# Kernel tuning notes

Measured on AMD Instinct MI355X. Metric: run time of the kernel, lower is better.

Reference implementation:

```python
import jax, jax.numpy as jnp
import numpy as np

N_NODES = 100000
N_EDGES = 1000000
D_IN = 128
D_H = 128
N_CLS = 16


def setup_inputs() -> dict:
    key = jax.random.key(0)
    ks = jax.random.split(key, 12)
    s_in = 1.0 / np.sqrt(D_IN)
    s_h = 1.0 / np.sqrt(D_H)
    s_2h = 1.0 / np.sqrt(2 * D_H)
    return {
        "x": jax.random.normal(ks[0], (N_NODES, D_IN), jnp.float32),
        "edge_index": jax.random.randint(ks[1], (2, N_EDGES), 0, N_NODES, jnp.int64),
        "W_l0": jax.random.normal(ks[2], (D_H, D_IN), jnp.float32) * s_in,
        "b_l0": jnp.zeros((D_H,), jnp.float32),
        "W_r0": jax.random.normal(ks[3], (D_H, D_IN), jnp.float32) * s_in,
        "W_l1": jax.random.normal(ks[4], (D_H, D_H), jnp.float32) * s_h,
        "b_l1": jnp.zeros((D_H,), jnp.float32),
        "W_r1": jax.random.normal(ks[5], (D_H, D_H), jnp.float32) * s_h,
        "W_c": jax.random.normal(ks[6], (D_H, 2 * D_H), jnp.float32) * s_2h,
        "b_c": jnp.zeros((D_H,), jnp.float32),
        "W_o": jax.random.normal(ks[7], (N_CLS, 2 * D_H), jnp.float32) * s_2h,
        "b_o": jnp.zeros((N_CLS,), jnp.float32),
    }


def _sage_conv(x, src, dst, W_l, b_l, W_r, num_nodes):
    # PyG SAGEConv (mean aggr): lin_l(mean of source-neighbor feats) + lin_r(x)
    msgs = x[src]  # [E, d] gather
    agg = jax.ops.segment_sum(msgs, dst, num_segments=num_nodes)
    cnt = jax.ops.segment_sum(jnp.ones((src.shape[0],), x.dtype), dst, num_segments=num_nodes)
    mean = agg / jnp.maximum(cnt, 1.0)[:, None]
    return mean @ W_l.T + b_l + x @ W_r.T


def reference(x, edge_index, W_l0, b_l0, W_r0, W_l1, b_l1, W_r1, W_c, b_c, W_o, b_o):
    src, dst = edge_index[0], edge_index[1]
    n = x.shape[0]
    for W_l, b_l, W_r in ((W_l0, b_l0, W_r0), (W_l1, b_l1, W_r1)):
        x_old = x
        h = jax.nn.relu(_sage_conv(x, src, dst, W_l, b_l, W_r, n))
        x = jnp.concatenate([x_old, h], axis=-1)  # [N, 2*hidden]
        x = jax.nn.relu(x @ W_c.T + b_c)
        # dropout: identity (eval mode)
    edge_feats = jnp.concatenate([x[src], x[dst]], axis=-1)  # [E, 2*hidden]
    return edge_feats @ W_o.T + b_o
```

## Files before the change

kernel.cpp:

```cpp
#include <hip/hip_runtime.h>
#include <hip/hip_bf16.h>

#define NN 100000
#define NE 1000000
#define D  128
#define NC 16

typedef short short8 __attribute__((ext_vector_type(8)));
typedef float f32x4  __attribute__((ext_vector_type(4)));
typedef unsigned int u32x4 __attribute__((ext_vector_type(4)));

__device__ __forceinline__ float bf2f(ushort u) {
  union { unsigned int i; float f; } v; v.i = ((unsigned int)u) << 16; return v.f;
}
__device__ __forceinline__ ushort f2bf(float f) {
  union { float f; unsigned int i; } v; v.f = f;
  unsigned int x = v.i;
  return (ushort)((x + 0x7FFFu + ((x >> 16) & 1u)) >> 16);
}

#define BSH 9
#define NBKT ((NN + 511) >> BSH)
#define MS_NBLK 256
#define MS_EPB ((NE + MS_NBLK - 1) / MS_NBLK)
#define CSR_CAP 8192

__global__ void sniff_k(const ushort* __restrict__ xr, const unsigned int* __restrict__ ei,
                        int* __restrict__ flags, int* __restrict__ bhist) {
  int t = threadIdx.x;
  if (t < NBKT) bhist[t] = 0;
  if (t != 0 || blockIdx.x != 0) return;
  int f32 = 0;
  for (int i = 0; i < 128; ++i) {
    unsigned int e = ((unsigned int)xr[i] >> 7) & 0xFFu;
    if (e < 97u || e > 157u) f32 = 1;
  }
  flags[0] = f32;
  unsigned int s = 0;
  for (int i = 1; i < 256; i += 2) s |= ei[i];
  flags[1] = (s == 0) ? 1 : 0;
}

__global__ __launch_bounds__(256) void convert_idx_k(
    const int* __restrict__ ei, const int* __restrict__ flags,
    int* __restrict__ idx, int* __restrict__ bhist) {
  __shared__ int h[NBKT];
  for (int t = threadIdx.x; t < NBKT; t += 256) h[t] = 0;
  __syncthreads();
  const int stride = 256 * 256;
  const int i64 = flags[1];
  for (int i = blockIdx.x * 256 + threadIdx.x; i < 2 * NE; i += stride) {
    int v = i64 ? ei[2 * i] : ei[i];
    v = v < 0 ? 0 : (v >= NN ? NN - 1 : v);
    idx[i] = v;
    if (i >= NE) atomicAdd(&h[v >> BSH], 1);
  }
  __syncthreads();
  for (int t = threadIdx.x; t < NBKT; t += 256) if (h[t]) atomicAdd(&bhist[t], h[t]);
}

__global__ void convert_x_k(const void* __restrict__ xin, const int* __restrict__ flags,
                            ushort* __restrict__ xb) {
  int i = blockIdx.x * blockDim.x + threadIdx.x;
  const int n4 = NN * D / 4;
  if (i >= n4) return;
  ushort4 o;
  if (flags[0]) {
    float4 v = ((const float4*)xin)[i];
    o.x = f2bf(v.x); o.y = f2bf(v.y); o.z = f2bf(v.z); o.w = f2bf(v.w);
  } else {
    o = ((const ushort4*)xin)[i];
  }
  ((ushort4*)xb)[i] = o;
}

struct WPtrs { const void* p[10]; };
#define WTOT 102800
__global__ void convert_w_k(WPtrs w, const int* __restrict__ flags, ushort* __restrict__ wb) {
  const int off[10] = {0, 16384, 32768, 49152, 65536, 98304, 102400, 102528, 102656, 102784};
  int i = blockIdx.x * blockDim.x + threadIdx.x;
  if (i >= WTOT) return;
  int seg = 0;
  #pragma unroll
  for (int s2 = 1; s2 < 10; ++s2) if (i >= off[s2]) seg = s2;
  int j = i - off[seg];
  wb[i] = flags[0] ? f2bf(((const float*)w.p[seg])[j]) : ((const ushort*)w.p[seg])[j];
}

__global__ __launch_bounds__(256) void scanb_k(const int* __restrict__ bhist,
                                               int* __restrict__ bstart,
                                               int* __restrict__ bcur) {
  __shared__ int tmp[256];
  const int t = threadIdx.x;
  int v = (t < NBKT) ? bhist[t] : 0;
  tmp[t] = v;
  __syncthreads();
  for (int s = 1; s < 256; s <<= 1) {
    int u = (t >= s) ? tmp[t - s] : 0;
    __syncthreads();
    tmp[t] += u;
    __syncthreads();
  }
  if (t < NBKT) {
    int ex = tmp[t] - v;
    bstart[t] = ex;
    bcur[t] = ex;
  }
  if (t == NBKT - 1) bstart[NBKT] = tmp[t];
}

__global__ __launch_bounds__(512) void msplit_k(const int* __restrict__ src,
                                                const int* __restrict__ dst,
                                                int* __restrict__ bcur,
                                                int2* __restrict__ ebuf) {
  __shared__ int2 ep[MS_EPB];
  __shared__ int hist[NBKT];
  __shared__ int gbase[NBKT];
  const int e0 = blockIdx.x * MS_EPB;
  int n = NE - e0; if (n > MS_EPB) n = MS_EPB;
  for (int t = threadIdx.x; t < NBKT; t += 512) hist[t] = 0;
  __syncthreads();
  for (int t = threadIdx.x; t < n; t += 512) {
    int s = src[e0 + t], d = dst[e0 + t];
    ep[t] = make_int2(s, d);
    atomicAdd(&hist[d >> BSH], 1);
  }
  __syncthreads();
  for (int t = threadIdx.x; t < NBKT; t += 512) {
    gbase[t] = atomicAdd(&bcur[t], hist[t]);
    hist[t] = 0;
  }
  __syncthreads();
  for (int t = threadIdx.x; t < n; t += 512) {
    int2 p = ep[t];
    int b = p.y >> BSH;
    int loc = atomicAdd(&hist[b], 1);
    ebuf[gbase[b] + loc] = p;
  }
}

__global__ __launch_bounds__(512) void csr_k(const int2* __restrict__ ebuf,
                                             const int* __restrict__ bstart,
                                             int* __restrict__ off,
                                             int* __restrict__ nbr) {
  __shared__ int cnt_s[512];
  __shared__ int ofs_s[512];
  __shared__ int lnbr[CSR_CAP];
  const int b = blockIdx.x;
  const int n0 = b << BSH;
  int nn = NN - n0; if (nn > 512) nn = 512;
  const int e0 = bstart[b], e1 = bstart[b + 1];
  const int n = e1 - e0;
  const int t = threadIdx.x;
  cnt_s[t] = 0;
  __syncthreads();
  for (int i = t; i < n; i += 512)
    atomicAdd(&cnt_s[ebuf[e0 + i].y - n0], 1);
  __syncthreads();
  int v = cnt_s[t];
  ofs_s[t] = v;
  __syncthreads();
  for (int s = 1; s < 512; s <<= 1) {
    int u = (t >= s) ? ofs_s[t - s] : 0;
    __syncthreads();
    ofs_s[t] += u;
    __syncthreads();
  }
  const int excl = ofs_s[t] - v;
  if (t < nn) off[n0 + t] = e0 + excl;
  if (b == gridDim.x - 1 && t == 0) off[NN] = e1;
  cnt_s[t] = excl;
  __syncthreads();
  if (n <= CSR_CAP) {
    for (int i = t; i < n; i += 512) {
      int2 p = ebuf[e0 + i];
      int loc = atomicAdd(&cnt_s[p.y - n0], 1);
      lnbr[loc] = p.x;
    }
    __syncthreads();
    for (int i = t; i < n; i += 512) nbr[e0 + i] = lnbr[i];
  } else {
    for (int i = t; i < n; i += 512) {
      int2 p = ebuf[e0 + i];
      int loc = atomicAdd(&cnt_s[p.y - n0], 1);
      nbr[e0 + loc] = p.x;
    }
  }
}

__global__ __launch_bounds__(256) void agg_k(
    const ushort* __restrict__ X, const int* __restrict__ nbr,
    const int* __restrict__ off, ushort* __restrict__ mean) {
  const int wave = threadIdx.x >> 6, lane = threadIdx.x & 63;
  const int node = blockIdx.x * 4 + wave;
  if (node >= NN) return;
  const int j0 = off[node], j1 = off[node + 1];
  const int g = lane >> 4, l15 = lane & 15;
  float a[8];
  #pragma unroll
  for (int k = 0; k < 8; ++k) a[k] = 0.f;
  int j = j0 + g;
  for (; j + 4 < j1; j += 8) {
    int s0 = nbr[j], s1 = nbr[j + 4];
    uint4 v0 = *(const uint4*)(X + (size_t)s0 * D + l15 * 8);
    uint4 v1 = *(const uint4*)(X + (size_t)s1 * D + l15 * 8);
    unsigned int w0[4] = {v0.x, v0.y, v0.z, v0.w};
    unsigned int w1[4] = {v1.x, v1.y, v1.z, v1.w};
    #pragma unroll
    for (int k = 0; k < 4; ++k) {
      union { unsigned int u; float f; } lo0, hi0, lo1, hi1;
      lo0.u = w0[k] << 16; hi0.u = w0[k] & 0xffff0000u;
      lo1.u = w1[k] << 16; hi1.u = w1[k] & 0xffff0000u;
      a[2 * k]     += lo0.f + lo1.f;
      a[2 * k + 1] += hi0.f + hi1.f;
    }
  }
  if (j < j1) {
    uint4 v0 = *(const uint4*)(X + (size_t)nbr[j] * D + l15 * 8);
    unsigned int w0[4] = {v0.x, v0.y, v0.z, v0.w};
    #pragma unroll
    for (int k = 0; k < 4; ++k) {
      union { unsigned int u; float f; } lo0, hi0;
      lo0.u = w0[k] << 16; hi0.u = w0[k] & 0xffff0000u;
      a[2 * k]     += lo0.f;
      a[2 * k + 1] += hi0.f;
    }
  }
  #pragma unroll
  for (int k = 0; k < 8; ++k) {
    a[k] += __shfl_xor(a[k], 16, 64);
    a[k] += __shfl_xor(a[k], 32, 64);
  }
  if (g == 0) {
    int deg = j1 - j0;
    float inv = 1.f / (float)(deg > 1 ? deg : 1);
    uint4 o;
    o.x = (unsigned int)f2bf(a[0] * inv) | ((unsigned int)f2bf(a[1] * inv) << 16);
    o.y = (unsigned int)f2bf(a[2] * inv) | ((unsigned int)f2bf(a[3] * inv) << 16);
    o.z = (unsigned int)f2bf(a[4] * inv) | ((unsigned int)f2bf(a[5] * inv) << 16);
    o.w = (unsigned int)f2bf(a[6] * inv) | ((unsigned int)f2bf(a[7] * inv) << 16);
    *(uint4*)(mean + (size_t)node * D + l15 * 8) = o;
  }
}

#define STAGE_W(Wp, ldwv)                                                      \
  __syncthreads();                                                             \
  _Pragma("unroll")                                                            \
  for (int it = 0; it < 8; ++it) {                                             \
    int combo = it * 4 + wave;                                                 \
    int cc = combo >> 2, kk = combo & 3;                                       \
    *(uint4*)(&wlds[(combo * 64 + lane) * 8]) =                                \
        *(const uint4*)((Wp) + (size_t)(cc * 16 + l15) * (ldwv) + kk * 32 + q * 8); \
  }                                                                            \
  __syncthreads();

#define MFMA_TERM(bfr)                                                         \
  _Pragma("unroll")                                                            \
  for (int ks = 0; ks < 4; ++ks)                                               \
    _Pragma("unroll")                                                          \
    for (int c = 0; c < 8; ++c) {                                              \
      short8 bf = *(const short8*)(&wlds[((c * 4 + ks) * 64 + lane) * 8]);     \
      acc[0][c] = __builtin_amdgcn_mfma_f32_16x16x32_bf16(bf, (bfr)[0][ks], acc[0][c], 0, 0, 0); \
      acc[1][c] = __builtin_amdgcn_mfma_f32_16x16x32_bf16(bf, (bfr)[1][ks], acc[1][c], 0, 0, 0); \
    }

__global__ __launch_bounds__(256, 2) void fused_layer_k(
    const ushort* __restrict__ MEAN, const ushort* __restrict__ X,
    const ushort* __restrict__ Wl, const ushort* __restrict__ Wr,
    const ushort* __restrict__ Wc,
    const ushort* __restrict__ bl, const ushort* __restrict__ bc,
    ushort* __restrict__ Y, int nrows)
{
  __shared__ ushort wlds[32 * 64 * 8];
  const int tid = threadIdx.x;
  const int wave = tid >> 6, lane = tid & 63;
  const int l15 = lane & 15, q = lane >> 4;
  const int nb = blockIdx.x * 128 + wave * 32;

  int r0 = nb + l15;      if (r0 > nrows - 1) r0 = nrows - 1;
  int r1 = nb + 16 + l15; if (r1 > nrows - 1) r1 = nrows - 1;

  short8 am[2][4], ax[2][4];
  #pragma unroll
  for (int ks = 0; ks < 4; ++ks) {
    am[0][ks] = *(const short8*)(MEAN + (size_t)r0 * D + ks * 32 + q * 8);
    am[1][ks] = *(const short8*)(MEAN + (size_t)r1 * D + ks * 32 + q * 8);
    ax[0][ks] = *(const short8*)(X    + (size_t)r0 * D + ks * 32 + q * 8);
    ax[1][ks] = *(const short8*)(X    + (size_t)r1 * D + ks * 32 + q * 8);
  }

  f32x4 acc[2][8];
  #pragma unroll
  for (int rt = 0; rt < 2; ++rt)
    #pragma unroll
    for (int c = 0; c < 8; ++c) acc[rt][c] = (f32x4){0.f, 0.f, 0.f, 0.f};

  STAGE_W(Wl, D);
  MFMA_TERM(am);
  STAGE_W(Wr, D);
  MFMA_TERM(ax);

  uint2 hp[2][8];
  #pragma unroll
  for (int c = 0; c < 8; ++c) {
    ushort4 bv = *(const ushort4*)(bl + c * 16 + q * 4);
    #pragma unroll
    for (int rt = 0; rt < 2; ++rt) {
      float v0 = acc[rt][c][0] + bf2f(bv.x); v0 = v0 > 0.f ? v0 : 0.f;
      float v1 = acc[rt][c][1] + bf2f(bv.y); v1 = v1 > 0.f ? v1 : 0.f;
      float v2 = acc[rt][c][2] + bf2f(bv.z); v2 = v2 > 0.f ? v2 : 0.f;
      float v3 = acc[rt][c][3] + bf2f(bv.w); v3 = v3 > 0.f ? v3 : 0.f;
      hp[rt][c].x = (unsigned int)f2bf(v0) | ((unsigned int)f2bf(v1) << 16);
      hp[rt][c].y = (unsigned int)f2bf(v2) | ((unsigned int)f2bf(v3) << 16);
    }
  }

  const int sl0 = l15 + 16 * ((2 * q) & 3);
  const int sl1 = l15 + 16 * ((2 * q + 1) & 3);
  const bool hi = (q >> 1) != 0;
  short8 hf[2][4];
  #pragma unroll
  for (int rt = 0; rt < 2; ++rt)
    #pragma unroll
    for (int ks = 0; ks < 4; ++ks) {
      unsigned int a0 = (unsigned int)__shfl((int)hp[rt][2 * ks].x,     sl0, 64);
      unsigned int a1 = (unsigned int)__shfl((int)hp[rt][2 * ks].y,     sl0, 64);
      unsigned int a2 = (unsigned int)__shfl((int)hp[rt][2 * ks].x,     sl1, 64);
      unsigned int a3 = (unsigned int)__shfl((int)hp[rt][2 * ks].y,     sl1, 64);
      unsigned int b0 = (unsigned int)__shfl((int)hp[rt][2 * ks + 1].x, sl0, 64);
      unsigned int b1 = (unsigned int)__shfl((int)hp[rt][2 * ks + 1].y, sl0, 64);
      unsigned int b2 = (unsigned int)__shfl((int)hp[rt][2 * ks + 1].x, sl1, 64);
      unsigned int b3 = (unsigned int)__shfl((int)hp[rt][2 * ks + 1].y, sl1, 64);
      u32x4 t;
      t.x = hi ? b0 : a0;
      t.y = hi ? b1 : a1;
      t.z = hi ? b2 : a2;
      t.w = hi ? b3 : a3;
      hf[rt][ks] = __builtin_bit_cast(short8, t);
    }

  #pragma unroll
  for (int rt = 0; rt < 2; ++rt)
    #pragma unroll
    for (int c = 0; c < 8; ++c) acc[rt][c] = (f32x4){0.f, 0.f, 0.f, 0.f};

  STAGE_W(Wc, 2 * D);
  MFMA_TERM(ax);
  STAGE_W(Wc + D, 2 * D);
  MFMA_TERM(hf);

  #pragma unroll
  for (int c = 0; c < 8; ++c) {
    ushort4 bv = *(const ushort4*)(bc + c * 16 + q * 4);
    #pragma unroll
    for (int rt = 0; rt < 2; ++rt) {
      int node = nb + rt * 16 + l15;
      if (node < nrows) {
        float v0 = acc[rt][c][0] + bf2f(bv.x); v0 = v0 > 0.f ? v0 : 0.f;
        float v1 = acc[rt][c][1] + bf2f(bv.y); v1 = v1 > 0.f ? v1 : 0.f;
        float v2 = acc[rt][c][2] + bf2f(bv.z); v2 = v2 > 0.f ? v2 : 0.f;
        float v3 = acc[rt][c][3] + bf2f(bv.w); v3 = v3 > 0.f ? v3 : 0.f;
        uint2 o;
        o.x = (unsigned int)f2bf(v0) | ((unsigned int)f2bf(v1) << 16);
        o.y = (unsigned int)f2bf(v2) | ((unsigned int)f2bf(v3) << 16);
        *(uint2*)(Y + (size_t)node * D + c * 16 + q * 4) = o;
      }
    }
  }
}

__global__ __launch_bounds__(256) void gemm_po(
    const ushort* __restrict__ X2, const ushort* __restrict__ Wo, float* __restrict__ P)
{
  const int tid = threadIdx.x, wave = tid >> 6, lane = tid & 63;
  const int l15 = lane & 15, q = lane >> 4;
  const int m0 = blockIdx.x * 64 + wave * 16;
  int row = m0 + l15; if (row > NN - 1) row = NN - 1;
  f32x4 acc[2] = {(f32x4){0.f,0.f,0.f,0.f}, (f32x4){0.f,0.f,0.f,0.f}};
  #pragma unroll
  for (int ks = 0; ks < 4; ++ks) {
    short8 af = *(const short8*)(X2 + (size_t)row * D + ks * 32 + q * 8);
    #pragma unroll
    for (int c = 0; c < 2; ++c) {
      short8 bf = *(const short8*)(Wo + (size_t)l15 * 256 + c * 128 + ks * 32 + q * 8);
      acc[c] = __builtin_amdgcn_mfma_f32_16x16x32_bf16(af, bf, acc[c], 0, 0, 0);
    }
  }
  #pragma unroll
  for (int c = 0; c < 2; ++c)
    #pragma unroll
    for (int r = 0; r < 4; ++r) {
      int orow = m0 + q * 4 + r;
      if (orow < NN) P[(size_t)orow * 32 + c * 16 + l15] = acc[c][r];
    }
}

__global__ __launch_bounds__(256) void edge_sum_k(
    const float* __restrict__ P, const int* __restrict__ src, const int* __restrict__ dst,
    const ushort* __restrict__ bo, const int* __restrict__ flags,
    void* __restrict__ outv, int E)
{
  int gid = blockIdx.x * blockDim.x + threadIdx.x;
  if (gid >= E * 4) return;
  int e = gid >> 2, cq = (gid & 3) * 4;
  int s = src[e], d = dst[e];
  float4 a = *(const float4*)(P + (size_t)s * 32 + cq);
  float4 b = *(const float4*)(P + (size_t)d * 32 + 16 + cq);
  float4 o;
  o.x = a.x + b.x + bf2f(bo[cq + 0]);
  o.y = a.y + b.y + bf2f(bo[cq + 1]);
  o.z = a.z + b.z + bf2f(bo[cq + 2]);
  o.w = a.w + b.w + bf2f(bo[cq + 3]);
  if (flags[0]) {
    ((float4*)outv)[gid] = o;
  } else {
    ushort4 u;
    u.x = f2bf(o.x); u.y = f2bf(o.y); u.z = f2bf(o.z); u.w = f2bf(o.w);
    ((ushort4*)outv)[gid] = u;
  }
}

extern "C" void kernel_launch(void* const* d_in, const int* in_sizes, int n_in,
                              void* d_out, int out_size, void* d_ws, size_t ws_size,
                              hipStream_t stream) {
  const void* x_in = d_in[0];
  const int*  ei   = (const int*)d_in[1];

  char* ws = (char*)d_ws;
  int*    idx   = (int*)(ws + 0);
  int*    bhist = (int*)(ws + 8000000);
  int*    flags = (int*)(ws + 8400000);
  ushort* wb    = (ushort*)(ws + 8400256);
  int*    off   = (int*)(ws + 8605856);
  int*    bstart= (int*)(ws + 9005872);
  int*    nbr   = (int*)(ws + 9405872);
  int*    bcur  = (int*)(ws + 13405872);
  ushort* buf1  = (ushort*)(ws + 13407440);
  ushort* buf2  = (ushort*)(ws + 39007440);
  ushort* dscr  = (ushort*)d_out;
  float*  P     = (float*)buf1;
  int2*   ebuf  = (int2*)buf1;

  int* src = idx;
  int* dst = idx + NE;

  ushort* Wl0 = wb + 0,      *Wr0 = wb + 16384, *Wl1 = wb + 32768, *Wr1 = wb + 49152;
  ushort* Wc  = wb + 65536,  *Wo  = wb + 98304;
  ushort* bl0 = wb + 102400, *bl1 = wb + 102528, *bc = wb + 102656, *bo = wb + 102784;

  WPtrs w;
  w.p[0] = d_in[2];  w.p[1] = d_in[4];  w.p[2] = d_in[5];  w.p[3] = d_in[7];
  w.p[4] = d_in[8];  w.p[5] = d_in[10]; w.p[6] = d_in[3];  w.p[7] = d_in[6];
  w.p[8] = d_in[9];  w.p[9] = d_in[11];

  const int gblocks = (NN + 127) / 128;
  const int n4 = NN * D / 4;
  const int agrid = (NN + 3) / 4;

  sniff_k<<<1, 256, 0, stream>>>((const ushort*)x_in, (const unsigned int*)ei, flags, bhist);
  convert_idx_k<<<256, 256, 0, stream>>>(ei, flags, idx, bhist);
  convert_x_k<<<(n4 + 255) / 256, 256, 0, stream>>>(x_in, flags, buf2);
  convert_w_k<<<(WTOT + 255) / 256, 256, 0, stream>>>(w, flags, wb);

  scanb_k<<<1, 256, 0, stream>>>(bhist, bstart, bcur);
  msplit_k<<<MS_NBLK, 512, 0, stream>>>(src, dst, bcur, ebuf);
  csr_k<<<NBKT, 512, 0, stream>>>(ebuf, bstart, off, nbr);

  agg_k<<<agrid, 256, 0, stream>>>(buf2, nbr, off, dscr);
  fused_layer_k<<<gblocks, 256, 0, stream>>>(dscr, buf2, Wl0, Wr0, Wc, bl0, bc, buf1, NN);

  agg_k<<<agrid, 256, 0, stream>>>(buf1, nbr, off, dscr);
  fused_layer_k<<<gblocks, 256, 0, stream>>>(dscr, buf1, Wl1, Wr1, Wc, bl1, bc, buf2, NN);

  gemm_po<<<(NN + 63) / 64, 256, 0, stream>>>(buf2, Wo, P);
  edge_sum_k<<<(4 * NE + 255) / 256, 256, 0, stream>>>(P, src, dst, bo, flags, d_out, NE);
}
```

Measured before the change: 441.3 us.

## Stage weights in half tiles and route hidden activations through LDS

Weight staging into LDS is split into two halves of output columns (16 KB instead of 32 KB per stage), so each matrix term takes two stage/sync/MFMA passes. The intermediate hidden activations are written to a padded LDS buffer and read back as MFMA operands, replacing the cross-lane shuffle transpose and its register arrays. This aims to lower register pressure and shuffle cost, and possibly change LDS use per block. In exchange it doubles the number of __syncthreads barriers and adds LDS write/read traffic for the hidden tile.

```diff
diff --git a/kernel.cpp b/kernel.cpp
--- a/kernel.cpp
+++ b/kernel.cpp
@@ -8,7 +8,6 @@
 
 typedef short short8 __attribute__((ext_vector_type(8)));
 typedef float f32x4  __attribute__((ext_vector_type(4)));
-typedef unsigned int u32x4 __attribute__((ext_vector_type(4)));
 
 __device__ __forceinline__ float bf2f(ushort u) {
   union { unsigned int i; float f; } v; v.i = ((unsigned int)u) << 16; return v.f;
@@ -243,26 +242,45 @@
   }
 }
 
-#define STAGE_W(Wp, ldwv)                                                      \
+#define STAGE_WH(Wp, ldwv, HALF)                                               \
   __syncthreads();                                                             \
   _Pragma("unroll")                                                            \
-  for (int it = 0; it < 8; ++it) {                                             \
+  for (int it = 0; it < 4; ++it) {                                             \
     int combo = it * 4 + wave;                                                 \
     int cc = combo >> 2, kk = combo & 3;                                       \
     *(uint4*)(&wlds[(combo * 64 + lane) * 8]) =                                \
-        *(const uint4*)((Wp) + (size_t)(cc * 16 + l15) * (ldwv) + kk * 32 + q * 8); \
+        *(const uint4*)((Wp) + (size_t)(((HALF) * 4 + cc) * 16 + l15) * (ldwv) + kk * 32 + q * 8); \
   }                                                                            \
   __syncthreads();
 
-#define MFMA_TERM(bfr)                                                         \
+#define MFMA_HALF(bfr, HALF)                                                   \
   _Pragma("unroll")                                                            \
   for (int ks = 0; ks < 4; ++ks)                                               \
     _Pragma("unroll")                                                          \
-    for (int c = 0; c < 8; ++c) {                                              \
-      short8 bf = *(const short8*)(&wlds[((c * 4 + ks) * 64 + lane) * 8]);     \
-      acc[0][c] = __builtin_amdgcn_mfma_f32_16x16x32_bf16(bf, (bfr)[0][ks], acc[0][c], 0, 0, 0); \
-      acc[1][c] = __builtin_amdgcn_mfma_f32_16x16x32_bf16(bf, (bfr)[1][ks], acc[1][c], 0, 0, 0); \
-    }
+    for (int cl = 0; cl < 4; ++cl) {                                           \
+      short8 bf = *(const short8*)(&wlds[((cl * 4 + ks) * 64 + lane) * 8]);    \
+      acc[0][(HALF) * 4 + cl] =                                                \
+          __builtin_amdgcn_mfma_f32_16x16x32_bf16(bf, (bfr)[0][ks], acc[0][(HALF) * 4 + cl], 0, 0, 0); \
+      acc[1][(HALF) * 4 + cl] =                                                \
+          __builtin_amdgcn_mfma_f32_16x16x32_bf16(bf, (bfr)[1][ks], acc[1][(HALF) * 4 + cl], 0, 0, 0); \
+    }
+
+#define MFMA_HHALF(HALF)                                                       \
+  _Pragma("unroll")                                                            \
+  for (int ks = 0; ks < 4; ++ks) {                                             \
+    short8 h0 = *(const short8*)(&hlds[hb0 + ks * 32 + q * 8]);                \
+    short8 h1 = *(const short8*)(&hlds[hb1 + ks * 32 + q * 8]);                \
+    _Pragma("unroll")                                                          \
+    for (int cl = 0; cl < 4; ++cl) {                                           \
+      short8 bf = *(const short8*)(&wlds[((cl * 4 + ks) * 64 + lane) * 8]);    \
+      acc[0][(HALF) * 4 + cl] =                                                \
+          __builtin_amdgcn_mfma_f32_16x16x32_bf16(bf, h0, acc[0][(HALF) * 4 + cl], 0, 0, 0); \
+      acc[1][(HALF) * 4 + cl] =                                                \
+          __builtin_amdgcn_mfma_f32_16x16x32_bf16(bf, h1, acc[1][(HALF) * 4 + cl], 0, 0, 0); \
+    }                                                                          \
+  }
+
+#define HLDW 132
 
 __global__ __launch_bounds__(256, 2) void fused_layer_k(
     const ushort* __restrict__ MEAN, const ushort* __restrict__ X,
@@ -271,7 +289,8 @@
     const ushort* __restrict__ bl, const ushort* __restrict__ bc,
     ushort* __restrict__ Y, int nrows)
 {
-  __shared__ ushort wlds[32 * 64 * 8];
+  __shared__ ushort wlds[16 * 64 * 8];
+  __shared__ ushort hlds[128 * HLDW];
   const int tid = threadIdx.x;
   const int wave = tid >> 6, lane = tid & 63;
   const int l15 = lane & 15, q = lane >> 4;
@@ -295,12 +314,11 @@
     #pragma unroll
     for (int c = 0; c < 8; ++c) acc[rt][c] = (f32x4){0.f, 0.f, 0.f, 0.f};
 
-  STAGE_W(Wl, D);
-  MFMA_TERM(am);
-  STAGE_W(Wr, D);
-  MFMA_TERM(ax);
-
-  uint2 hp[2][8];
+  STAGE_WH(Wl, D, 0);  MFMA_HALF(am, 0);
+  STAGE_WH(Wl, D, 1);  MFMA_HALF(am, 1);
+  STAGE_WH(Wr, D, 0);  MFMA_HALF(ax, 0);
+  STAGE_WH(Wr, D, 1);  MFMA_HALF(ax, 1);
+
   #pragma unroll
   for (int c = 0; c < 8; ++c) {
     ushort4 bv = *(const ushort4*)(bl + c * 16 + q * 4);
@@ -310,44 +328,26 @@
       float v1 = acc[rt][c][1] + bf2f(bv.y); v1 = v1 > 0.f ? v1 : 0.f;
       float v2 = acc[rt][c][2] + bf2f(bv.z); v2 = v2 > 0.f ? v2 : 0.f;
       float v3 = acc[rt][c][3] + bf2f(bv.w); v3 = v3 > 0.f ? v3 : 0.f;
-      hp[rt][c].x = (unsigned int)f2bf(v0) | ((unsigned int)f2bf(v1) << 16);
-      hp[rt][c].y = (unsigned int)f2bf(v2) | ((unsigned int)f2bf(v3) << 16);
-    }
-  }
-
-  const int sl0 = l15 + 16 * ((2 * q) & 3);
-  const int sl1 = l15 + 16 * ((2 * q + 1) & 3);
-  const bool hi = (q >> 1) != 0;
-  short8 hf[2][4];
+      uint2 o;
+      o.x = (unsigned int)f2bf(v0) | ((unsigned int)f2bf(v1) << 16);
+      o.y = (unsigned int)f2bf(v2) | ((unsigned int)f2bf(v3) << 16);
+      int nl = wave * 32 + rt * 16 + l15;
+      *(uint2*)(&hlds[nl * HLDW + c * 16 + q * 4]) = o;
+    }
+  }
+
   #pragma unroll
   for (int rt = 0; rt < 2; ++rt)
     #pragma unroll
-    for (int ks = 0; ks < 4; ++ks) {
-      unsigned int a0 = (unsigned int)__shfl((int)hp[rt][2 * ks].x,     sl0, 64);
-      unsigned int a1 = (unsigned int)__shfl((int)hp[rt][2 * ks].y,     sl0, 64);
-      unsigned int a2 = (unsigned int)__shfl((int)hp[rt][2 * ks].x,     sl1, 64);
-      unsigned int a3 = (unsigned int)__shfl((int)hp[rt][2 * ks].y,     sl1, 64);
-      unsigned int b0 = (unsigned int)__shfl((int)hp[rt][2 * ks + 1].x, sl0, 64);
-      unsigned int b1 = (unsigned int)__shfl((int)hp[rt][2 * ks + 1].y, sl0, 64);
-      unsigned int b2 = (unsigned int)__shfl((int)hp[rt][2 * ks + 1].x, sl1, 64);
-      unsigned int b3 = (unsigned int)__shfl((int)hp[rt][2 * ks + 1].y, sl1, 64);
-      u32x4 t;
-      t.x = hi ? b0 : a0;
-      t.y = hi ? b1 : a1;
-      t.z = hi ? b2 : a2;
-      t.w = hi ? b3 : a3;
-      hf[rt][ks] = __builtin_bit_cast(short8, t);
-    }
-
-  #pragma unroll
-  for (int rt = 0; rt < 2; ++rt)
-    #pragma unroll
     for (int c = 0; c < 8; ++c) acc[rt][c] = (f32x4){0.f, 0.f, 0.f, 0.f};
 
-  STAGE_W(Wc, 2 * D);
-  MFMA_TERM(ax);
-  STAGE_W(Wc + D, 2 * D);
-  MFMA_TERM(hf);
+  const int hb0 = (wave * 32 + l15) * HLDW;
+  const int hb1 = (wave * 32 + 16 + l15) * HLDW;
+
+  STAGE_WH(Wc, 2 * D, 0);      MFMA_HALF(ax, 0);
+  STAGE_WH(Wc, 2 * D, 1);      MFMA_HALF(ax, 1);
+  STAGE_WH(Wc + D, 2 * D, 0);  MFMA_HHALF(0);
+  STAGE_WH(Wc + D, 2 * D, 1);  MFMA_HHALF(1);
 
   #pragma unroll
   for (int c = 0; c < 8; ++c) {
```

New measurement: 436.1 us. No clear change (-1.2%).
